# Kernel tuning notes

Hardware: AMD Instinct MI355X
Metric: run time of the kernel (lower is better)

The kernel has to match this reference:

```python
import jax, jax.numpy as jnp
import numpy as np

B, CIN, COUT, H, W = 16, 128, 128, 64, 64
K1, K2, DIL = 3, 3, 1
PAD0 = DIL * (K1 - 1) // 2
PAD1 = DIL * (K2 - 1) // 2
L = H * W


def setup_inputs() -> dict:
    key = jax.random.key(0)
    k1, k2, k3, k4, k5 = jax.random.split(key, 5)
    x = jax.random.normal(k1, (B, CIN, H, W), dtype=jnp.float32)
    # binary per-pixel mask over kernel taps, broadcast over batch*channels
    mask = (jax.random.uniform(k2, (1, K1 * K2, L)) < 0.5).astype(jnp.float32)
    fan_in = CIN * K1 * K2
    bound = 1.0 / np.sqrt(fan_in)
    weight = jax.random.uniform(k3, (COUT, CIN, K1, K2), jnp.float32, -bound, bound)
    mask_weight = jax.random.uniform(k4, (COUT, K1, K2), jnp.float32, -bound, bound)
    bias = jax.random.uniform(k5, (COUT,), jnp.float32, -bound, bound)
    return {"x": x, "mask": mask, "weight": weight, "mask_weight": mask_weight, "bias": bias}


def reference(x, mask, weight, mask_weight, bias):
    # im2col: [B, CIN*K1*K2, H, W]; channel ordering (cin, k1, k2) matches torch unfold
    patches = jax.lax.conv_general_dilated_patches(
        x, (K1, K2), (1, 1), [(PAD0, PAD0), (PAD1, PAD1)], rhs_dilation=(DIL, DIL))
    p = patches.reshape(B, CIN, K1 * K2, L)
    p = p * mask[:, None, :, :]          # mask [1, K, L] broadcasts over B and CIN
    p = p.reshape(B, CIN * K1 * K2, L)
    out = jnp.einsum('ok,bkl->bol', weight.reshape(COUT, -1), p)
    out = out + bias[None, :, None]
    out = out + jnp.einsum('ok,mkl->mol', mask_weight.reshape(COUT, -1), mask)
    return out.reshape(B, COUT, H, W)
```

## Files before the change

### kernel.cpp

```cpp
#include <hip/hip_runtime.h>
#include <stdint.h>

#define B_    16
#define CIN_  128
#define COUT_ 128
#define H_    64
#define W_    64
#define L_    4096
#define KK_   1152

typedef unsigned short u16;
typedef __bf16 bf16x8 __attribute__((ext_vector_type(8)));
typedef float  floatx4 __attribute__((ext_vector_type(4)));
typedef uint32_t u32x4 __attribute__((ext_vector_type(4)));

typedef const __attribute__((address_space(1))) uint32_t* gptr_t;
typedef __attribute__((address_space(3))) uint32_t*       lptr_t;

__device__ __forceinline__ void async_copy16(const void* g, void* l) {
    __builtin_amdgcn_global_load_lds((gptr_t)g, (lptr_t)l, 16, 0, 0);
}

__device__ __forceinline__ u16 f2bf(float f) {
    uint32_t u = __builtin_bit_cast(uint32_t, f);
    uint32_t r = u + 0x7FFFu + ((u >> 16) & 1u);
    return (u16)(r >> 16);
}

__global__ void lmc_prep_kernel(const float* __restrict__ mask, const float* __restrict__ mw,
                                const float* __restrict__ bias, const float* __restrict__ w,
                                float* __restrict__ mb, u16* __restrict__ wb2) {
    const int bid = blockIdx.x, tid = threadIdx.x;
    if (bid < 128) {
        const int o = bid;
        float m[9];
        #pragma unroll
        for (int k = 0; k < 9; ++k) m[k] = mw[o * 9 + k];
        const float bs = bias[o];
        for (int l = tid; l < L_; l += 256) {
            float s = bs;
            #pragma unroll
            for (int k = 0; k < 9; ++k) s += m[k] * mask[k * L_ + l];
            mb[o * L_ + l] = s;
        }
    } else {
        const int base = (bid - 128) * 2304;
        #pragma unroll
        for (int i = 0; i < 9; ++i) {
            const int e = base + i * 256 + tid;
            const int k = e >> 14;
            const int rem = e & 16383;
            const int o = rem >> 7, c = rem & 127;
            wb2[e] = f2bf(w[(size_t)o * KK_ + c * 9 + k]);
        }
    }
}

__global__ __launch_bounds__(512, 2)
void lmc_gemm_kernel(const float* __restrict__ x, const u16* __restrict__ wb2,
                     const float* __restrict__ mask, const float* __restrict__ mb,
                     float* __restrict__ out) {
    __shared__ u16 W_lds[396 * 128];
    __shared__ u16 A_lds[3][128 * 64];

    const int flat    = blockIdx.x;
    const int logical = (flat & 7) * 32 + (flat >> 3);
    const int b       = logical >> 4;
    const int lt      = logical & 15;
    const int Y       = lt * 4;
    const int l0      = lt * 256;

    const int tid  = threadIdx.x;
    const int lane = tid & 63;
    const int wv   = tid >> 6;
    const int wm   = (wv >> 2) * 64;
    const int wn   = (wv & 3) * 64;
    const int lrow = lane & 15;
    const int quad = lane >> 4;

    if (tid < 192) {
        const int h  = tid >> 4;
        const int px = (h >> 1) * 66 + ((h & 1) ? 65 : 0);
        const uint4 z = {0u, 0u, 0u, 0u};
        *reinterpret_cast<uint4*>((char*)W_lds + px * 256 + (tid & 15) * 16) = z;
    }
    {
        const int cg  = lane >> 4;
        const int x0  = (lane & 15) * 4;
        const int cb  = wv;
        const int cbase = cb * 16 + cg * 4;
        const int d     = cb * 2 + (cg >> 1);
        const int half8 = (cg & 1) * 8;
        const float* xc = x + ((size_t)(b * CIN_ + cbase) * L_) + x0;

        #pragma unroll
        for (int wy = 0; wy < 6; ++wy) {
            const int y   = Y - 1 + wy;
            const int px0 = wy * 66 + x0 + 1;
            if (y >= 0 && y <= 63) {
                const float* xr = xc + y * 64;
                float4 v0 = *reinterpret_cast<const float4*>(xr);
                float4 v1 = *reinterpret_cast<const float4*>(xr + L_);
                float4 v2 = *reinterpret_cast<const float4*>(xr + 2 * L_);
                float4 v3 = *reinterpret_cast<const float4*>(xr + 3 * L_);
                const float* p0 = (const float*)&v0;
                const float* p1 = (const float*)&v1;
                const float* p2 = (const float*)&v2;
                const float* p3 = (const float*)&v3;
                #pragma unroll
                for (int j = 0; j < 4; ++j) {
                    const int px   = px0 + j;
                    const int slot = d ^ (px & 7);
                    uint2 pk;
                    pk.x = (uint32_t)f2bf(p0[j]) | ((uint32_t)f2bf(p1[j]) << 16);
                    pk.y = (uint32_t)f2bf(p2[j]) | ((uint32_t)f2bf(p3[j]) << 16);
                    *reinterpret_cast<uint2*>((char*)W_lds + px * 256 + slot * 16 + half8) = pk;
                }
            } else {
                const uint2 z2 = {0u, 0u};
                #pragma unroll
                for (int j = 0; j < 4; ++j) {
                    const int px   = px0 + j;
                    const int slot = d ^ (px & 7);
                    *reinterpret_cast<uint2*>((char*)W_lds + px * 256 + slot * 16 + half8) = z2;
                }
            }
        }
    }

    int pix0[4];
    uint64_t bits = 0;
    #pragma unroll
    for (int j = 0; j < 4; ++j) {
        const int ll = wn + j * 16 + lrow;
        pix0[j] = ((ll >> 6) + 1) * 66 + (ll & 63) + 1;
        const int lg = l0 + ll;
        #pragma unroll
        for (int k = 0; k < 9; ++k)
            if (mask[k * L_ + lg] != 0.0f) bits |= (1ull << (k * 4 + j));
    }

    const char* wb2_c = (const char*)wb2;
    char* A_c = (char*)A_lds;
    const int ao  = (lane >> 3);
    const int ach = (lane & 7) ^ (ao & 7);
    const int aoff0 = (8 * wv + ao) * 256 + ach * 16;
    async_copy16(wb2_c + aoff0,               A_c + wv * 1024);
    async_copy16(wb2_c + aoff0 + 16384,       A_c + wv * 1024 + 8192);
    async_copy16(wb2_c + 128 + aoff0,         A_c + 16384 + wv * 1024);
    async_copy16(wb2_c + 128 + aoff0 + 16384, A_c + 16384 + wv * 1024 + 8192);

    floatx4 acc[4][4];
    #pragma unroll
    for (int i = 0; i < 4; ++i)
        #pragma unroll
        for (int j = 0; j < 4; ++j)
            acc[i][j] = (floatx4){0.f, 0.f, 0.f, 0.f};

    asm volatile("s_waitcnt vmcnt(2) lgkmcnt(0)" ::: "memory");
    __builtin_amdgcn_s_barrier();
    asm volatile("" ::: "memory");

    int bufr = 0;
    int bufw = 2;
    for (int g = 0; g < 18; ++g) {
        const int k = g >> 1;

        if (g < 16) {
            const int gn   = g + 2;
            const int koff = (gn >> 1) * 32768 + (gn & 1) * 128;
            char* dstb = A_c + bufw * 16384;
            async_copy16(wb2_c + koff + aoff0,         dstb + wv * 1024);
            async_copy16(wb2_c + koff + aoff0 + 16384, dstb + wv * 1024 + 8192);
        }

        const int sh = (k / 3 - 1) * 66 + (k % 3) - 1;
        uint32_t kp[4];
        #pragma unroll
        for (int j = 0; j < 4; ++j)
            kp[j] = 0u - (uint32_t)((bits >> (k * 4 + j)) & 1ull);

        const u16* Ac = (const u16*)(A_c + bufr * 16384);

        #pragma unroll
        for (int ksl = 0; ksl < 2; ++ksl) {
            const int ksg = (g & 1) * 2 + ksl;
            bf16x8 af[4], bf[4];
            #pragma unroll
            for (int i = 0; i < 4; ++i) {
                const int orow = wm + i * 16 + lrow;
                const int slot = (ksl * 4 + quad) ^ (orow & 7);
                af[i] = *reinterpret_cast<const bf16x8*>(&Ac[orow * 64 + slot * 8]);
            }
            #pragma unroll
            for (int j = 0; j < 4; ++j) {
                const int pix  = pix0[j] + sh;
                const int slot = (ksg * 4 + quad) ^ (pix & 7);
                bf16x8 v = *reinterpret_cast<const bf16x8*>(&W_lds[pix * 128 + slot * 8]);
                u32x4 t = __builtin_bit_cast(u32x4, v);
                t &= kp[j];
                bf[j] = __builtin_bit_cast(bf16x8, t);
            }
            __builtin_amdgcn_s_setprio(1);
            #pragma unroll
            for (int i = 0; i < 4; ++i)
                #pragma unroll
                for (int j = 0; j < 4; ++j)
                    acc[i][j] = __builtin_amdgcn_mfma_f32_16x16x32_bf16(
                        af[i], bf[j], acc[i][j], 0, 0, 0);
            __builtin_amdgcn_s_setprio(0);
        }

        if (g < 16) {
            asm volatile("s_waitcnt vmcnt(2)" ::: "memory");
            __builtin_amdgcn_s_barrier();
            asm volatile("" ::: "memory");
        } else if (g == 16) {
            asm volatile("s_waitcnt vmcnt(0)" ::: "memory");
            __builtin_amdgcn_s_barrier();
            asm volatile("" ::: "memory");
        }
        bufr = (bufr == 2) ? 0 : bufr + 1;
        bufw = (bufw == 2) ? 0 : bufw + 1;
    }

    #pragma unroll
    for (int i = 0; i < 4; ++i) {
        #pragma unroll
        for (int j = 0; j < 4; ++j) {
            const int l = l0 + wn + j * 16 + lrow;
            #pragma unroll
            for (int r = 0; r < 4; ++r) {
                const int o = wm + i * 16 + quad * 4 + r;
                out[((size_t)b * COUT_ + o) * L_ + l] = acc[i][j][r] + mb[o * L_ + l];
            }
        }
    }
}

extern "C" void kernel_launch(void* const* d_in, const int* in_sizes, int n_in,
                              void* d_out, int out_size, void* d_ws, size_t ws_size,
                              hipStream_t stream) {
    const float* x      = (const float*)d_in[0];
    const float* mask   = (const float*)d_in[1];
    const float* weight = (const float*)d_in[2];
    const float* mw     = (const float*)d_in[3];
    const float* bias   = (const float*)d_in[4];
    float* out = (float*)d_out;

    char* ws = (char*)d_ws;
    u16*   wb2 = (u16*)ws;
    float* mb  = (float*)(ws + 294912);

    lmc_prep_kernel<<<192, 256, 0, stream>>>(mask, mw, bias, weight, mb, wb2);
    lmc_gemm_kernel<<<256, 512, 0, stream>>>(x, wb2, mask, mb, out);
}
```

Baseline: 118.5 us.

## Halve GEMM tile to 128 pixels with 256-thread blocks and unpadded halo

Each block now covers two image rows (128 pixels) with 4 waves instead of four rows with 8 waves, doubling the grid to 512 blocks. The LDS input window drops the left/right zero-padding columns, and horizontal edge taps are masked through the per-pixel tap bits instead. The weight pipeline changes from triple-buffered 64-wide K slices to double-buffered 32-wide slices with a full vmcnt(0) barrier each step. The aim is lower LDS use and more resident blocks per CU for better occupancy and load balance. In exchange, the halo overhead per block rises and there are twice as many barriers with less prefetch depth.

```diff
diff --git a/kernel.cpp b/kernel.cpp
--- a/kernel.cpp
+++ b/kernel.cpp
@@ -56,99 +56,99 @@
     }
 }
 
-__global__ __launch_bounds__(512, 2)
+__global__ __launch_bounds__(256, 2)
 void lmc_gemm_kernel(const float* __restrict__ x, const u16* __restrict__ wb2,
                      const float* __restrict__ mask, const float* __restrict__ mb,
                      float* __restrict__ out) {
-    __shared__ u16 W_lds[396 * 128];
-    __shared__ u16 A_lds[3][128 * 64];
+    __shared__ u16 W_lds[256 * 128];
+    __shared__ u16 A_lds[2][128 * 32];
 
     const int flat    = blockIdx.x;
-    const int logical = (flat & 7) * 32 + (flat >> 3);
-    const int b       = logical >> 4;
-    const int lt      = logical & 15;
-    const int Y       = lt * 4;
-    const int l0      = lt * 256;
+    const int logical = (flat & 7) * 64 + (flat >> 3);
+    const int b       = logical >> 5;
+    const int lt      = logical & 31;
+    const int Y       = lt * 2;
+    const int l0      = lt * 128;
 
     const int tid  = threadIdx.x;
     const int lane = tid & 63;
     const int wv   = tid >> 6;
-    const int wm   = (wv >> 2) * 64;
-    const int wn   = (wv & 3) * 64;
+    const int wm   = (wv >> 1) * 64;
+    const int wn   = (wv & 1) * 64;
     const int lrow = lane & 15;
     const int quad = lane >> 4;
 
-    if (tid < 192) {
-        const int h  = tid >> 4;
-        const int px = (h >> 1) * 66 + ((h & 1) ? 65 : 0);
-        const uint4 z = {0u, 0u, 0u, 0u};
-        *reinterpret_cast<uint4*>((char*)W_lds + px * 256 + (tid & 15) * 16) = z;
-    }
     {
-        const int cg  = lane >> 4;
-        const int x0  = (lane & 15) * 4;
-        const int cb  = wv;
-        const int cbase = cb * 16 + cg * 4;
-        const int d     = cb * 2 + (cg >> 1);
-        const int half8 = (cg & 1) * 8;
+        const int cg    = lane >> 4;
+        const int x0    = (lane & 15) * 4;
+        const int cbase = wv * 32 + cg * 8;
+        const int d     = wv * 4 + cg;
         const float* xc = x + ((size_t)(b * CIN_ + cbase) * L_) + x0;
 
         #pragma unroll
-        for (int wy = 0; wy < 6; ++wy) {
-            const int y   = Y - 1 + wy;
-            const int px0 = wy * 66 + x0 + 1;
+        for (int wy = 0; wy < 4; ++wy) {
+            const int y = Y - 1 + wy;
             if (y >= 0 && y <= 63) {
                 const float* xr = xc + y * 64;
-                float4 v0 = *reinterpret_cast<const float4*>(xr);
-                float4 v1 = *reinterpret_cast<const float4*>(xr + L_);
-                float4 v2 = *reinterpret_cast<const float4*>(xr + 2 * L_);
-                float4 v3 = *reinterpret_cast<const float4*>(xr + 3 * L_);
-                const float* p0 = (const float*)&v0;
-                const float* p1 = (const float*)&v1;
-                const float* p2 = (const float*)&v2;
-                const float* p3 = (const float*)&v3;
+                float4 v[8];
                 #pragma unroll
-                for (int j = 0; j < 4; ++j) {
-                    const int px   = px0 + j;
+                for (int cr = 0; cr < 8; ++cr)
+                    v[cr] = *reinterpret_cast<const float4*>(xr + (size_t)cr * L_);
+                #pragma unroll
+                for (int jj = 0; jj < 4; ++jj) {
+                    const int px   = wy * 64 + x0 + jj;
                     const int slot = d ^ (px & 7);
-                    uint2 pk;
-                    pk.x = (uint32_t)f2bf(p0[j]) | ((uint32_t)f2bf(p1[j]) << 16);
-                    pk.y = (uint32_t)f2bf(p2[j]) | ((uint32_t)f2bf(p3[j]) << 16);
-                    *reinterpret_cast<uint2*>((char*)W_lds + px * 256 + slot * 16 + half8) = pk;
+                    uint4 pk;
+                    pk.x = (uint32_t)f2bf(((const float*)&v[0])[jj]) |
+                           ((uint32_t)f2bf(((const float*)&v[1])[jj]) << 16);
+                    pk.y = (uint32_t)f2bf(((const float*)&v[2])[jj]) |
+                           ((uint32_t)f2bf(((const float*)&v[3])[jj]) << 16);
+                    pk.z = (uint32_t)f2bf(((const float*)&v[4])[jj]) |
+                           ((uint32_t)f2bf(((const float*)&v[5])[jj]) << 16);
+                    pk.w = (uint32_t)f2bf(((const float*)&v[6])[jj]) |
+                           ((uint32_t)f2bf(((const float*)&v[7])[jj]) << 16);
+                    *reinterpret_cast<uint4*>((char*)W_lds + px * 256 + slot * 16) = pk;
                 }
             } else {
-                const uint2 z2 = {0u, 0u};
+                const uint4 z = {0u, 0u, 0u, 0u};
                 #pragma unroll
-                for (int j = 0; j < 4; ++j) {
-                    const int px   = px0 + j;
+                for (int jj = 0; jj < 4; ++jj) {
+                    const int px   = wy * 64 + x0 + jj;
                     const int slot = d ^ (px & 7);
-                    *reinterpret_cast<uint2*>((char*)W_lds + px * 256 + slot * 16 + half8) = z2;
+                    *reinterpret_cast<uint4*>((char*)W_lds + px * 256 + slot * 16) = z;
                 }
             }
         }
     }
+
+    const int arow0 = 16 * (wv * 2)     + (lane >> 2);
+    const int arow1 = 16 * (wv * 2 + 1) + (lane >> 2);
+    const int aslx  = (lane & 3) ^ ((lane >> 2) & 3);
+    const uint32_t aoffA0 = (uint32_t)(arow0 * 256 + aslx * 16);
+    const uint32_t aoffA1 = (uint32_t)(arow1 * 256 + aslx * 16);
+
+    const char* wb2_c = (const char*)wb2;
+    char* A_c = (char*)A_lds;
+
+    async_copy16(wb2_c + aoffA0, A_c + wv * 2048);
+    async_copy16(wb2_c + aoffA1, A_c + wv * 2048 + 1024);
 
     int pix0[4];
     uint64_t bits = 0;
     #pragma unroll
     for (int j = 0; j < 4; ++j) {
         const int ll = wn + j * 16 + lrow;
-        pix0[j] = ((ll >> 6) + 1) * 66 + (ll & 63) + 1;
+        const int xx = ll & 63;
+        pix0[j] = ((ll >> 6) + 1) * 64 + xx;
         const int lg = l0 + ll;
         #pragma unroll
-        for (int k = 0; k < 9; ++k)
-            if (mask[k * L_ + lg] != 0.0f) bits |= (1ull << (k * 4 + j));
-    }
-
-    const char* wb2_c = (const char*)wb2;
-    char* A_c = (char*)A_lds;
-    const int ao  = (lane >> 3);
-    const int ach = (lane & 7) ^ (ao & 7);
-    const int aoff0 = (8 * wv + ao) * 256 + ach * 16;
-    async_copy16(wb2_c + aoff0,               A_c + wv * 1024);
-    async_copy16(wb2_c + aoff0 + 16384,       A_c + wv * 1024 + 8192);
-    async_copy16(wb2_c + 128 + aoff0,         A_c + 16384 + wv * 1024);
-    async_copy16(wb2_c + 128 + aoff0 + 16384, A_c + 16384 + wv * 1024 + 8192);
+        for (int k = 0; k < 9; ++k) {
+            const int dx  = k % 3 - 1;
+            const bool ok = (xx + dx >= 0) && (xx + dx < 64) &&
+                            (mask[k * L_ + lg] != 0.0f);
+            if (ok) bits |= (1ull << (k * 4 + j));
+        }
+    }
 
     floatx4 acc[4][4];
     #pragma unroll
@@ -157,71 +157,66 @@
         for (int j = 0; j < 4; ++j)
             acc[i][j] = (floatx4){0.f, 0.f, 0.f, 0.f};
 
-    asm volatile("s_waitcnt vmcnt(2) lgkmcnt(0)" ::: "memory");
+    asm volatile("s_waitcnt vmcnt(0) lgkmcnt(0)" ::: "memory");
     __builtin_amdgcn_s_barrier();
     asm volatile("" ::: "memory");
 
-    int bufr = 0;
-    int bufw = 2;
-    for (int g = 0; g < 18; ++g) {
-        const int k = g >> 1;
-
-        if (g < 16) {
-            const int gn   = g + 2;
-            const int koff = (gn >> 1) * 32768 + (gn & 1) * 128;
-            char* dstb = A_c + bufw * 16384;
-            async_copy16(wb2_c + koff + aoff0,         dstb + wv * 1024);
-            async_copy16(wb2_c + koff + aoff0 + 16384, dstb + wv * 1024 + 8192);
-        }
-
-        const int sh = (k / 3 - 1) * 66 + (k % 3) - 1;
+    int buf = 0;
+    for (int s = 0; s < 36; ++s) {
+        const int k = s >> 2;
+        const int q = s & 3;
+
+        if (s < 35) {
+            const int sn   = s + 1;
+            const int koff = (sn >> 2) * 32768 + (sn & 3) * 64;
+            char* dstb = A_c + (buf ^ 1) * 8192;
+            async_copy16(wb2_c + koff + aoffA0, dstb + wv * 2048);
+            async_copy16(wb2_c + koff + aoffA1, dstb + wv * 2048 + 1024);
+        }
+
+        const int dy = k / 3 - 1;
+        const int dx = k - (k / 3) * 3 - 1;
+        const int sh = dy * 64 + dx;
+
         uint32_t kp[4];
         #pragma unroll
         for (int j = 0; j < 4; ++j)
             kp[j] = 0u - (uint32_t)((bits >> (k * 4 + j)) & 1ull);
 
-        const u16* Ac = (const u16*)(A_c + bufr * 16384);
-
-        #pragma unroll
-        for (int ksl = 0; ksl < 2; ++ksl) {
-            const int ksg = (g & 1) * 2 + ksl;
-            bf16x8 af[4], bf[4];
+        const u16* Ac = (const u16*)(A_c + buf * 8192);
+
+        bf16x8 af[4], bf[4];
+        #pragma unroll
+        for (int i = 0; i < 4; ++i) {
+            const int orow = wm + i * 16 + lrow;
+            const int slot = quad ^ (lrow & 3);
+            af[i] = *reinterpret_cast<const bf16x8*>(&Ac[orow * 32 + slot * 8]);
+        }
+        #pragma unroll
+        for (int j = 0; j < 4; ++j) {
+            int p = pix0[j] + sh;
+            p = (p < 0) ? 0 : p;
+            const int slot = (q * 4 + quad) ^ (p & 7);
+            bf16x8 v = *reinterpret_cast<const bf16x8*>(&W_lds[p * 128 + slot * 8]);
+            u32x4 t = __builtin_bit_cast(u32x4, v);
+            t &= kp[j];
+            bf[j] = __builtin_bit_cast(bf16x8, t);
+        }
+        __builtin_amdgcn_s_setprio(1);
+        #pragma unroll
+        for (int i = 0; i < 4; ++i)
             #pragma unroll
-            for (int i = 0; i < 4; ++i) {
-                const int orow = wm + i * 16 + lrow;
-                const int slot = (ksl * 4 + quad) ^ (orow & 7);
-                af[i] = *reinterpret_cast<const bf16x8*>(&Ac[orow * 64 + slot * 8]);
-            }
-            #pragma unroll
-            for (int j = 0; j < 4; ++j) {
-                const int pix  = pix0[j] + sh;
-                const int slot = (ksg * 4 + quad) ^ (pix & 7);
-                bf16x8 v = *reinterpret_cast<const bf16x8*>(&W_lds[pix * 128 + slot * 8]);
-                u32x4 t = __builtin_bit_cast(u32x4, v);
-                t &= kp[j];
-                bf[j] = __builtin_bit_cast(bf16x8, t);
-            }
-            __builtin_amdgcn_s_setprio(1);
-            #pragma unroll
-            for (int i = 0; i < 4; ++i)
-                #pragma unroll
-                for (int j = 0; j < 4; ++j)
-                    acc[i][j] = __builtin_amdgcn_mfma_f32_16x16x32_bf16(
-                        af[i], bf[j], acc[i][j], 0, 0, 0);
-            __builtin_amdgcn_s_setprio(0);
-        }
-
-        if (g < 16) {
-            asm volatile("s_waitcnt vmcnt(2)" ::: "memory");
-            __builtin_amdgcn_s_barrier();
-            asm volatile("" ::: "memory");
-        } else if (g == 16) {
+            for (int j = 0; j < 4; ++j)
+                acc[i][j] = __builtin_amdgcn_mfma_f32_16x16x32_bf16(
+                    af[i], bf[j], acc[i][j], 0, 0, 0);
+        __builtin_amdgcn_s_setprio(0);
+
+        if (s < 35) {
             asm volatile("s_waitcnt vmcnt(0)" ::: "memory");
             __builtin_amdgcn_s_barrier();
             asm volatile("" ::: "memory");
         }
-        bufr = (bufr == 2) ? 0 : bufr + 1;
-        bufw = (bufw == 2) ? 0 : bufw + 1;
+        buf ^= 1;
     }
 
     #pragma unroll
@@ -253,5 +248,5 @@
     float* mb  = (float*)(ws + 294912);
 
     lmc_prep_kernel<<<192, 256, 0, stream>>>(mask, mw, bias, weight, mb, wb2);
-    lmc_gemm_kernel<<<256, 512, 0, stream>>>(x, wb2, mask, mb, out);
-}
+    lmc_gemm_kernel<<<512, 256, 0, stream>>>(x, wb2, mask, mb, out);
+}
```

Measured after the change: 122.7 us. +3.6%, slower.

## Remove halo columns from input tile and use double-buffered full-K weight stages

Applied to the files above, without the earlier changes.

Drops the zero-padded halo columns from the LDS input tile (66-wide rows become 64-wide). Horizontal boundary handling moves into the per-pixel mask bits, and pixel indices are clamped. The weight pipeline changes from a triple buffer of half-K slices (18 steps) to a double buffer of full 128-channel taps (9 steps). This halves the number of barriers and removes the halo-zeroing stores. In exchange each barrier now waits for all outstanding loads (vmcnt(0)), which reduces prefetch depth.

```diff
diff --git a/kernel.cpp b/kernel.cpp
--- a/kernel.cpp
+++ b/kernel.cpp
@@ -60,8 +60,8 @@
 void lmc_gemm_kernel(const float* __restrict__ x, const u16* __restrict__ wb2,
                      const float* __restrict__ mask, const float* __restrict__ mb,
                      float* __restrict__ out) {
-    __shared__ u16 W_lds[396 * 128];
-    __shared__ u16 A_lds[3][128 * 64];
+    __shared__ u16 W_lds[384 * 128];
+    __shared__ u16 A_lds[2][128 * 128];
 
     const int flat    = blockIdx.x;
     const int logical = (flat & 7) * 32 + (flat >> 3);
@@ -78,25 +78,18 @@
     const int lrow = lane & 15;
     const int quad = lane >> 4;
 
-    if (tid < 192) {
-        const int h  = tid >> 4;
-        const int px = (h >> 1) * 66 + ((h & 1) ? 65 : 0);
-        const uint4 z = {0u, 0u, 0u, 0u};
-        *reinterpret_cast<uint4*>((char*)W_lds + px * 256 + (tid & 15) * 16) = z;
-    }
     {
-        const int cg  = lane >> 4;
-        const int x0  = (lane & 15) * 4;
-        const int cb  = wv;
-        const int cbase = cb * 16 + cg * 4;
-        const int d     = cb * 2 + (cg >> 1);
+        const int cg    = lane >> 4;
+        const int x0    = (lane & 15) * 4;
+        const int cbase = wv * 16 + cg * 4;
+        const int d     = wv * 2 + (cg >> 1);
         const int half8 = (cg & 1) * 8;
         const float* xc = x + ((size_t)(b * CIN_ + cbase) * L_) + x0;
 
         #pragma unroll
         for (int wy = 0; wy < 6; ++wy) {
             const int y   = Y - 1 + wy;
-            const int px0 = wy * 66 + x0 + 1;
+            const int px0 = wy * 64 + x0;
             if (y >= 0 && y <= 63) {
                 const float* xr = xc + y * 64;
                 float4 v0 = *reinterpret_cast<const float4*>(xr);
@@ -128,27 +121,35 @@
         }
     }
 
+    const char* wb2_c = (const char*)wb2;
+    char* A_c = (char*)A_lds;
+    uint32_t aoff[4];
+    #pragma unroll
+    for (int ti = 0; ti < 4; ++ti) {
+        const int r  = 16 * wv + 4 * ti + (lane >> 4);
+        const int sc = (lane & 15) ^ (r & 7);
+        aoff[ti] = (uint32_t)(r * 256 + sc * 16);
+    }
+    #pragma unroll
+    for (int ti = 0; ti < 4; ++ti)
+        async_copy16(wb2_c + aoff[ti], A_c + (wv * 4 + ti) * 1024);
+
     int pix0[4];
     uint64_t bits = 0;
     #pragma unroll
     for (int j = 0; j < 4; ++j) {
         const int ll = wn + j * 16 + lrow;
-        pix0[j] = ((ll >> 6) + 1) * 66 + (ll & 63) + 1;
+        const int xx = ll & 63;
+        pix0[j] = ((ll >> 6) + 1) * 64 + xx;
         const int lg = l0 + ll;
         #pragma unroll
-        for (int k = 0; k < 9; ++k)
-            if (mask[k * L_ + lg] != 0.0f) bits |= (1ull << (k * 4 + j));
-    }
-
-    const char* wb2_c = (const char*)wb2;
-    char* A_c = (char*)A_lds;
-    const int ao  = (lane >> 3);
-    const int ach = (lane & 7) ^ (ao & 7);
-    const int aoff0 = (8 * wv + ao) * 256 + ach * 16;
-    async_copy16(wb2_c + aoff0,               A_c + wv * 1024);
-    async_copy16(wb2_c + aoff0 + 16384,       A_c + wv * 1024 + 8192);
-    async_copy16(wb2_c + 128 + aoff0,         A_c + 16384 + wv * 1024);
-    async_copy16(wb2_c + 128 + aoff0 + 16384, A_c + 16384 + wv * 1024 + 8192);
+        for (int k = 0; k < 9; ++k) {
+            const int dx  = k % 3 - 1;
+            const bool ok = (xx + dx >= 0) && (xx + dx < 64) &&
+                            (mask[k * L_ + lg] != 0.0f);
+            if (ok) bits |= (1ull << (k * 4 + j));
+        }
+    }
 
     floatx4 acc[4][4];
     #pragma unroll
@@ -157,46 +158,46 @@
         for (int j = 0; j < 4; ++j)
             acc[i][j] = (floatx4){0.f, 0.f, 0.f, 0.f};
 
-    asm volatile("s_waitcnt vmcnt(2) lgkmcnt(0)" ::: "memory");
+    asm volatile("s_waitcnt vmcnt(0) lgkmcnt(0)" ::: "memory");
     __builtin_amdgcn_s_barrier();
     asm volatile("" ::: "memory");
 
-    int bufr = 0;
-    int bufw = 2;
-    for (int g = 0; g < 18; ++g) {
-        const int k = g >> 1;
-
-        if (g < 16) {
-            const int gn   = g + 2;
-            const int koff = (gn >> 1) * 32768 + (gn & 1) * 128;
-            char* dstb = A_c + bufw * 16384;
-            async_copy16(wb2_c + koff + aoff0,         dstb + wv * 1024);
-            async_copy16(wb2_c + koff + aoff0 + 16384, dstb + wv * 1024 + 8192);
-        }
-
-        const int sh = (k / 3 - 1) * 66 + (k % 3) - 1;
+    for (int k = 0; k < 9; ++k) {
+        if (k < 8) {
+            const int koff = (k + 1) * 32768;
+            char* dstb = A_c + ((k + 1) & 1) * 32768;
+            #pragma unroll
+            for (int ti = 0; ti < 4; ++ti)
+                async_copy16(wb2_c + koff + aoff[ti], dstb + (wv * 4 + ti) * 1024);
+        }
+
+        const int dy = k / 3 - 1;
+        const int dx = k - (k / 3) * 3 - 1;
+        const int sh = dy * 64 + dx;
+
         uint32_t kp[4];
         #pragma unroll
         for (int j = 0; j < 4; ++j)
             kp[j] = 0u - (uint32_t)((bits >> (k * 4 + j)) & 1ull);
 
-        const u16* Ac = (const u16*)(A_c + bufr * 16384);
-
-        #pragma unroll
-        for (int ksl = 0; ksl < 2; ++ksl) {
-            const int ksg = (g & 1) * 2 + ksl;
+        const u16* Ac = (const u16*)(A_c + (k & 1) * 32768);
+
+        #pragma unroll
+        for (int ks = 0; ks < 4; ++ks) {
             bf16x8 af[4], bf[4];
             #pragma unroll
             for (int i = 0; i < 4; ++i) {
                 const int orow = wm + i * 16 + lrow;
-                const int slot = (ksl * 4 + quad) ^ (orow & 7);
-                af[i] = *reinterpret_cast<const bf16x8*>(&Ac[orow * 64 + slot * 8]);
+                const int slot = (ks * 4 + quad) ^ (orow & 7);
+                af[i] = *reinterpret_cast<const bf16x8*>(&Ac[orow * 128 + slot * 8]);
             }
             #pragma unroll
             for (int j = 0; j < 4; ++j) {
-                const int pix  = pix0[j] + sh;
-                const int slot = (ksg * 4 + quad) ^ (pix & 7);
-                bf16x8 v = *reinterpret_cast<const bf16x8*>(&W_lds[pix * 128 + slot * 8]);
+                int p = pix0[j] + sh;
+                p = (p < 0) ? 0 : p;
+                p = (p > 383) ? 383 : p;
+                const int slot = (ks * 4 + quad) ^ (p & 7);
+                bf16x8 v = *reinterpret_cast<const bf16x8*>(&W_lds[p * 128 + slot * 8]);
                 u32x4 t = __builtin_bit_cast(u32x4, v);
                 t &= kp[j];
                 bf[j] = __builtin_bit_cast(bf16x8, t);
@@ -211,17 +212,11 @@
             __builtin_amdgcn_s_setprio(0);
         }
 
-        if (g < 16) {
-            asm volatile("s_waitcnt vmcnt(2)" ::: "memory");
-            __builtin_amdgcn_s_barrier();
-            asm volatile("" ::: "memory");
-        } else if (g == 16) {
+        if (k < 8) {
             asm volatile("s_waitcnt vmcnt(0)" ::: "memory");
             __builtin_amdgcn_s_barrier();
             asm volatile("" ::: "memory");
         }
-        bufr = (bufr == 2) ? 0 : bufr + 1;
-        bufw = (bufw == 2) ? 0 : bufw + 1;
     }
 
     #pragma unroll
```

Result: no change. 117.4 us (-0.9%).
